# Performance work log

Measured on AMD Instinct MI355X. Metric: run time of the kernel, lower is better.

## Reference

```python
import jax, jax.numpy as jnp
import numpy as np

H = 1024   # hidden_size
V = 32000  # output_size (vocab)
S = 4096   # encoder seq_len
L = 1      # n_layers


def setup_inputs() -> dict:
    key = jax.random.key(0)
    ks = jax.random.split(key, 12)
    scale = 0.02
    return {
        "word_input": jax.random.randint(ks[0], (1,), 0, V),
        "last_hidden": jax.random.normal(ks[1], (L, 1, H), jnp.float32),
        "encoder_hiddens": jax.random.normal(ks[2], (S, 1, H), jnp.float32),
        "embedding": jax.random.normal(ks[3], (V, H), jnp.float32) * scale,
        "w_ih": jax.random.normal(ks[4], (3 * H, H), jnp.float32) * scale,
        "w_hh": jax.random.normal(ks[5], (3 * H, H), jnp.float32) * scale,
        "b_ih": jax.random.normal(ks[6], (3 * H,), jnp.float32) * scale,
        "b_hh": jax.random.normal(ks[7], (3 * H,), jnp.float32) * scale,
        "attn_w": jax.random.normal(ks[8], (H, H), jnp.float32) * scale,
        "attn_b": jax.random.normal(ks[9], (H,), jnp.float32) * scale,
        "out_w": jax.random.normal(ks[10], (V, 2 * H), jnp.float32) * scale,
        "out_b": jax.random.normal(ks[11], (V,), jnp.float32) * scale,
    }


def reference(word_input, last_hidden, encoder_hiddens, embedding,
              w_ih, w_hh, b_ih, b_hh, attn_w, attn_b, out_w, out_b):
    h_dim = embedding.shape[1]
    # embedding lookup -> GRU single step (PyTorch GRU cell math)
    x = embedding[word_input[0]]            # [H]
    h0 = last_hidden[0, 0]                  # [H]
    gx = w_ih @ x + b_ih                    # [3H]
    gh = w_hh @ h0 + b_hh                   # [3H]
    r = jax.nn.sigmoid(gx[:h_dim] + gh[:h_dim])
    z = jax.nn.sigmoid(gx[h_dim:2 * h_dim] + gh[h_dim:2 * h_dim])
    n = jnp.tanh(gx[2 * h_dim:] + r * gh[2 * h_dim:])
    h = (1.0 - z) * n + z * h0              # rnn_output / new hidden [H]
    # Bahdanau-style scores: dot(hidden, attn(enc_i)) for all i, batched
    enc = encoder_hiddens[:, 0, :]          # [S, H]
    scores = (enc @ attn_w.T + attn_b) @ h  # [S]
    attn = jax.nn.softmax(scores)           # [S]
    context = attn @ enc                    # [H]
    output = jnp.concatenate([h, context]) @ out_w.T + out_b  # [V]
    return (output[None, :], h[None, None, :], attn[None, None, :])
```

## Files before the change

### kernel.cpp

```cpp
#include <hip/hip_runtime.h>
#include <cstddef>

#define Hn 1024
#define Vn 32000
#define Sn 4096
#define CSHIFT 20.0f

__device__ __forceinline__ float wave_reduce_sum(float v) {
#pragma unroll
    for (int o = 32; o > 0; o >>= 1) v += __shfl_down(v, o, 64);
    return v;
}


__device__ __forceinline__ void out_h_rows(const float* __restrict__ out_w,
                                           const float* __restrict__ out_b,
                                           const float* __restrict__ ws_h,
                                           float* __restrict__ out,
                                           int row_base, int t)
{
    __shared__ float c[Hn];
    ((float4*)c)[t] = ((const float4*)ws_h)[t];
    __syncthreads();
    const int wv = t >> 6, lane = t & 63;
    const int row = row_base + wv;
    const float* w = out_w + (size_t)row * (2 * Hn);
    float acc = 0.f;
#pragma unroll
    for (int k = 0; k < 4; ++k) {
        const int idx = k * 256 + lane * 4;
        const float4 w4 = *(const float4*)(w + idx);
        acc += w4.x * c[idx] + w4.y * c[idx + 1] + w4.z * c[idx + 2] + w4.w * c[idx + 3];
    }
    acc = wave_reduce_sum(acc);
    if (lane == 0) out[row] = acc + out_b[row];
}

__global__ __launch_bounds__(256) void k_gru(const int* __restrict__ word,
                                             const float* __restrict__ emb,
                                             const float* __restrict__ h0,
                                             const float* __restrict__ w_ih,
                                             const float* __restrict__ w_hh,
                                             const float* __restrict__ b_ih,
                                             const float* __restrict__ b_hh,
                                             float* __restrict__ ws_h,
                                             float* __restrict__ ws_ctx,
                                             float* __restrict__ ws_denom,
                                             float* __restrict__ out_h)
{
    const int k = blockIdx.x;
    const int t = threadIdx.x;

    if (k == 0) {
#pragma unroll
        for (int i = 0; i < 4; ++i) ws_ctx[t + i * 256] = 0.f;
        if (t == 0) ws_denom[0] = 0.f;
    }

    const float* x = emb + (size_t)word[0] * Hn;
    const float4 xv = ((const float4*)x)[t];
    const float4 hv = ((const float4*)h0)[t];

    float acc[6];
    const float* rows[6] = {
        w_ih + (size_t)k * Hn, w_ih + (size_t)(k + Hn) * Hn, w_ih + (size_t)(k + 2 * Hn) * Hn,
        w_hh + (size_t)k * Hn, w_hh + (size_t)(k + Hn) * Hn, w_hh + (size_t)(k + 2 * Hn) * Hn
    };
#pragma unroll
    for (int g = 0; g < 6; ++g) {
        const float4 w = ((const float4*)rows[g])[t];
        const float4 vv = (g < 3) ? xv : hv;
        acc[g] = w.x * vv.x + w.y * vv.y + w.z * vv.z + w.w * vv.w;
    }

    __shared__ float red[6][4];
    const int wv = t >> 6, lane = t & 63;
#pragma unroll
    for (int g = 0; g < 6; ++g) {
        const float s = wave_reduce_sum(acc[g]);
        if (lane == 0) red[g][wv] = s;
    }
    __syncthreads();
    if (t == 0) {
        float g0 = red[0][0] + red[0][1] + red[0][2] + red[0][3] + b_ih[k];
        float g1 = red[1][0] + red[1][1] + red[1][2] + red[1][3] + b_ih[k + Hn];
        float g2 = red[2][0] + red[2][1] + red[2][2] + red[2][3] + b_ih[k + 2 * Hn];
        float g3 = red[3][0] + red[3][1] + red[3][2] + red[3][3] + b_hh[k];
        float g4 = red[4][0] + red[4][1] + red[4][2] + red[4][3] + b_hh[k + Hn];
        float g5 = red[5][0] + red[5][1] + red[5][2] + red[5][3] + b_hh[k + 2 * Hn];
        float r = 1.f / (1.f + expf(-(g0 + g3)));
        float z = 1.f / (1.f + expf(-(g1 + g4)));
        float n = tanhf(g2 + r * g5);
        float hk = (1.f - z) * n + z * h0[k];
        ws_h[k]  = hk;
        out_h[k] = hk;
    }
}

__global__ __launch_bounds__(256) void k_a(const float* __restrict__ attn_w,
                                           const float* __restrict__ ws_h,
                                           float* __restrict__ v,
                                           const float* __restrict__ out_w,
                                           const float* __restrict__ out_b,
                                           float* __restrict__ out)
{
    const int t = threadIdx.x, bid = blockIdx.x;
    if (bid < 64) {
        const int tj = t >> 4, tk = t & 15;
        const int k = bid * 16 + tk;
        float acc = 0.f;
        for (int j = tj; j < Hn; j += 16)
            acc += attn_w[(size_t)j * Hn + k] * ws_h[j];
        __shared__ float p[16][17];
        p[tj][tk] = acc;
        __syncthreads();
        if (t < 16) {
            float s = 0.f;
#pragma unroll
            for (int j = 0; j < 16; ++j) s += p[j][t];
            v[bid * 16 + t] = s;
        }
    } else {
        out_h_rows(out_w, out_b, ws_h, out, (bid - 64) * 4, t);
    }
}

__global__ __launch_bounds__(256) void k_sctx(const float* __restrict__ enc,
                                              const float* __restrict__ ws_v,
                                              float* __restrict__ escore,
                                              float* __restrict__ ctx,
                                              float* __restrict__ denom,
                                              const float* __restrict__ ws_h,
                                              const float* __restrict__ out_w,
                                              const float* __restrict__ out_b,
                                              float* __restrict__ out)
{
    const int t = threadIdx.x, bid = blockIdx.x;
    if (bid < 128) {
        __shared__ float rows[4][Hn];
        __shared__ float vsh[Hn];
        __shared__ float esl[4];
        const int wv = t >> 6, lane = t & 63;
        const int s0 = bid * 32;

        ((float4*)vsh)[t] = ((const float4*)ws_v)[t];

        float4 acc = make_float4(0.f, 0.f, 0.f, 0.f);
        float dsum = 0.f;

        for (int g = 0; g < 8; ++g) {
            __syncthreads();
            const float* erow = enc + (size_t)(s0 + g * 4) * Hn;
#pragma unroll
            for (int r = 0; r < 4; ++r)
                ((float4*)rows[r])[t] = ((const float4*)(erow + (size_t)r * Hn))[t];
            __syncthreads();

            float a = 0.f;
#pragma unroll
            for (int k = 0; k < 4; ++k) {
                const int idx = k * 256 + lane * 4;
                const float4 e = *(const float4*)&rows[wv][idx];
                a += e.x * vsh[idx] + e.y * vsh[idx + 1] + e.z * vsh[idx + 2] + e.w * vsh[idx + 3];
            }
            a = wave_reduce_sum(a);
            if (lane == 0) {
                const float ev = expf(a - CSHIFT);
                esl[wv] = ev;
                escore[s0 + g * 4 + wv] = ev;
            }
            __syncthreads();

            const float e0 = esl[0], e1 = esl[1], e2 = esl[2], e3 = esl[3];
            dsum += e0 + e1 + e2 + e3;
            const float4 r0 = ((const float4*)rows[0])[t];
            const float4 r1 = ((const float4*)rows[1])[t];
            const float4 r2 = ((const float4*)rows[2])[t];
            const float4 r3 = ((const float4*)rows[3])[t];
            acc.x += e0 * r0.x + e1 * r1.x + e2 * r2.x + e3 * r3.x;
            acc.y += e0 * r0.y + e1 * r1.y + e2 * r2.y + e3 * r3.y;
            acc.z += e0 * r0.z + e1 * r1.z + e2 * r2.z + e3 * r3.z;
            acc.w += e0 * r0.w + e1 * r1.w + e2 * r2.w + e3 * r3.w;
        }
        atomicAdd(&ctx[t * 4],     acc.x);
        atomicAdd(&ctx[t * 4 + 1], acc.y);
        atomicAdd(&ctx[t * 4 + 2], acc.z);
        atomicAdd(&ctx[t * 4 + 3], acc.w);
        if (t == 0) atomicAdd(denom, dsum);
    } else {
        out_h_rows(out_w, out_b, ws_h, out, 10668 + (bid - 128) * 4, t);
    }
}

__global__ __launch_bounds__(256) void k_red(const float* __restrict__ escore,
                                             const float* __restrict__ denom,
                                             float* __restrict__ out_attn,
                                             const float* __restrict__ ws_h,
                                             const float* __restrict__ out_w,
                                             const float* __restrict__ out_b,
                                             float* __restrict__ out)
{
    const int t = threadIdx.x, bid = blockIdx.x;
    if (bid < 4) {
        const float inv = 1.f / denom[0];
        const int s = bid * 1024 + t * 4;
        const float4 e = *(const float4*)(escore + s);
        *(float4*)(out_attn + s) = make_float4(e.x * inv, e.y * inv, e.z * inv, e.w * inv);
    } else {
        out_h_rows(out_w, out_b, ws_h, out, 21336 + (bid - 4) * 4, t);
    }
}

__global__ __launch_bounds__(256) void k_tail(const float* __restrict__ out_w,
                                              const float* __restrict__ ws_ctx,
                                              const float* __restrict__ denom,
                                              float* __restrict__ out)
{
    __shared__ float c[Hn];
    const int t = threadIdx.x;
    const float inv = 1.f / denom[0];
    ((float4*)c)[t] = ((const float4*)ws_ctx)[t];
    __syncthreads();
    const int wv = t >> 6, lane = t & 63;
    const int row = blockIdx.x * 4 + wv;
    const float* w = out_w + (size_t)row * (2 * Hn) + Hn;
    float acc = 0.f;
#pragma unroll
    for (int k = 0; k < 4; ++k) {
        const int idx = k * 256 + lane * 4;
        const float4 w4 = *(const float4*)(w + idx);
        acc += w4.x * c[idx] + w4.y * c[idx + 1] + w4.z * c[idx + 2] + w4.w * c[idx + 3];
    }
    acc = wave_reduce_sum(acc);
    if (lane == 0) out[row] += acc * inv;
}

extern "C" void kernel_launch(void* const* d_in, const int* in_sizes, int n_in,
                              void* d_out, int out_size, void* d_ws, size_t ws_size,
                              hipStream_t stream) {
    const int*   word   = (const int*)d_in[0];
    const float* h_last = (const float*)d_in[1];
    const float* enc    = (const float*)d_in[2];
    const float* emb    = (const float*)d_in[3];
    const float* w_ih   = (const float*)d_in[4];
    const float* w_hh   = (const float*)d_in[5];
    const float* b_ih   = (const float*)d_in[6];
    const float* b_hh   = (const float*)d_in[7];
    const float* attn_w = (const float*)d_in[8];
    const float* out_w  = (const float*)d_in[10];
    const float* out_b  = (const float*)d_in[11];
    float* out = (float*)d_out;
    float* ws  = (float*)d_ws;

    float* ws_h      = ws;
    float* ws_ctx    = ws + 1024;
    float* ws_v      = ws + 2048;
    float* ws_escore = ws + 3072;
    float* ws_denom  = ws + 7168;
    float* out_h     = out + Vn;
    float* out_attn  = out + Vn + Hn;

    k_gru<<<Hn, 256, 0, stream>>>(word, emb, h_last, w_ih, w_hh, b_ih, b_hh,
                                  ws_h, ws_ctx, ws_denom, out_h);
    k_a<<<64 + 2667, 256, 0, stream>>>(attn_w, ws_h, ws_v, out_w, out_b, out);
    k_sctx<<<128 + 2667, 256, 0, stream>>>(enc, ws_v, ws_escore, ws_ctx, ws_denom,
                                           ws_h, out_w, out_b, out);
    k_red<<<4 + 2666, 256, 0, stream>>>(ws_escore, ws_denom, out_attn,
                                        ws_h, out_w, out_b, out);
    k_tail<<<Vn / 4, 256, 0, stream>>>(out_w, ws_ctx, ws_denom, out);
}
```

Measured before the change: 95.21 us.

## Merge attention, score/context and normalize kernels into one with atomic-counter dependencies

Three launches (attn projection, score+context, softmax normalize), each padded with out_w h-half rows, become a single kernel. Ordering between the stages now comes from global atomic counters with spin-waits instead of kernel boundaries. The aim is to remove two launch gaps and let the out_w h-half GEMV fill the GPU alongside the dependent attention stages. Spin-waiting blocks assume the producer blocks (lower block IDs) are already resident, which carries a deadlock/ordering risk that relies on in-order dispatch.

```diff
diff --git a/kernel.cpp b/kernel.cpp
--- a/kernel.cpp
+++ b/kernel.cpp
@@ -12,29 +12,20 @@
     return v;
 }
 
-
-__device__ __forceinline__ void out_h_rows(const float* __restrict__ out_w,
-                                           const float* __restrict__ out_b,
-                                           const float* __restrict__ ws_h,
-                                           float* __restrict__ out,
-                                           int row_base, int t)
-{
-    __shared__ float c[Hn];
-    ((float4*)c)[t] = ((const float4*)ws_h)[t];
-    __syncthreads();
-    const int wv = t >> 6, lane = t & 63;
-    const int row = row_base + wv;
-    const float* w = out_w + (size_t)row * (2 * Hn);
-    float acc = 0.f;
-#pragma unroll
-    for (int k = 0; k < 4; ++k) {
-        const int idx = k * 256 + lane * 4;
-        const float4 w4 = *(const float4*)(w + idx);
-        acc += w4.x * c[idx] + w4.y * c[idx + 1] + w4.z * c[idx + 2] + w4.w * c[idx + 3];
-    }
-    acc = wave_reduce_sum(acc);
-    if (lane == 0) out[row] = acc + out_b[row];
-}
+__device__ __forceinline__ void block_signal(int* cnt, int t) {
+    __threadfence();
+    __syncthreads();
+    if (t == 0) __hip_atomic_fetch_add(cnt, 1, __ATOMIC_RELEASE, __HIP_MEMORY_SCOPE_AGENT);
+}
+__device__ __forceinline__ void block_wait(const int* cnt, int target, int t) {
+    if (t == 0) {
+        while (__hip_atomic_load(cnt, __ATOMIC_ACQUIRE, __HIP_MEMORY_SCOPE_AGENT) < target)
+            __builtin_amdgcn_s_sleep(4);
+    }
+    __syncthreads();
+    __threadfence();
+}
+
 
 __global__ __launch_bounds__(256) void k_gru(const int* __restrict__ word,
                                              const float* __restrict__ emb,
@@ -46,6 +37,7 @@
                                              float* __restrict__ ws_h,
                                              float* __restrict__ ws_ctx,
                                              float* __restrict__ ws_denom,
+                                             int*   __restrict__ ws_cnt,
                                              float* __restrict__ out_h)
 {
     const int k = blockIdx.x;
@@ -54,7 +46,7 @@
     if (k == 0) {
 #pragma unroll
         for (int i = 0; i < 4; ++i) ws_ctx[t + i * 256] = 0.f;
-        if (t == 0) ws_denom[0] = 0.f;
+        if (t == 0) { ws_denom[0] = 0.f; ws_cnt[0] = 0; ws_cnt[1] = 0; }
     }
 
     const float* x = emb + (size_t)word[0] * Hn;
@@ -97,51 +89,44 @@
     }
 }
 
-__global__ __launch_bounds__(256) void k_a(const float* __restrict__ attn_w,
-                                           const float* __restrict__ ws_h,
-                                           float* __restrict__ v,
-                                           const float* __restrict__ out_w,
-                                           const float* __restrict__ out_b,
-                                           float* __restrict__ out)
+__global__ __launch_bounds__(256) void k_mid(const float* __restrict__ attn_w,
+                                             const float* __restrict__ enc,
+                                             const float* __restrict__ ws_h,
+                                             float* __restrict__ ws_v,
+                                             float* __restrict__ escore,
+                                             float* __restrict__ ctx,
+                                             float* __restrict__ denom,
+                                             int*   __restrict__ cnt,
+                                             float* __restrict__ out_attn,
+                                             const float* __restrict__ out_w,
+                                             const float* __restrict__ out_b,
+                                             float* __restrict__ out)
 {
+    __shared__ float smem[5128];
     const int t = threadIdx.x, bid = blockIdx.x;
+    const int wv = t >> 6, lane = t & 63;
+
     if (bid < 64) {
         const int tj = t >> 4, tk = t & 15;
         const int k = bid * 16 + tk;
         float acc = 0.f;
         for (int j = tj; j < Hn; j += 16)
             acc += attn_w[(size_t)j * Hn + k] * ws_h[j];
-        __shared__ float p[16][17];
-        p[tj][tk] = acc;
+        smem[tj * 17 + tk] = acc;
         __syncthreads();
         if (t < 16) {
             float s = 0.f;
 #pragma unroll
-            for (int j = 0; j < 16; ++j) s += p[j][t];
-            v[bid * 16 + t] = s;
+            for (int j = 0; j < 16; ++j) s += smem[j * 17 + t];
+            ws_v[bid * 16 + t] = s;
         }
-    } else {
-        out_h_rows(out_w, out_b, ws_h, out, (bid - 64) * 4, t);
-    }
-}
-
-__global__ __launch_bounds__(256) void k_sctx(const float* __restrict__ enc,
-                                              const float* __restrict__ ws_v,
-                                              float* __restrict__ escore,
-                                              float* __restrict__ ctx,
-                                              float* __restrict__ denom,
-                                              const float* __restrict__ ws_h,
-                                              const float* __restrict__ out_w,
-                                              const float* __restrict__ out_b,
-                                              float* __restrict__ out)
-{
-    const int t = threadIdx.x, bid = blockIdx.x;
-    if (bid < 128) {
-        __shared__ float rows[4][Hn];
-        __shared__ float vsh[Hn];
-        __shared__ float esl[4];
-        const int wv = t >> 6, lane = t & 63;
-        const int s0 = bid * 32;
+        block_signal(&cnt[0], t);
+    } else if (bid < 192) {
+        block_wait(&cnt[0], 64, t);
+        float* rows = smem;
+        float* vsh  = smem + 4096;
+        float* esl  = smem + 5120;
+        const int s0 = (bid - 64) * 32;
 
         ((float4*)vsh)[t] = ((const float4*)ws_v)[t];
 
@@ -153,14 +138,14 @@
             const float* erow = enc + (size_t)(s0 + g * 4) * Hn;
 #pragma unroll
             for (int r = 0; r < 4; ++r)
-                ((float4*)rows[r])[t] = ((const float4*)(erow + (size_t)r * Hn))[t];
+                ((float4*)(rows + r * Hn))[t] = ((const float4*)(erow + (size_t)r * Hn))[t];
             __syncthreads();
 
             float a = 0.f;
 #pragma unroll
             for (int k = 0; k < 4; ++k) {
                 const int idx = k * 256 + lane * 4;
-                const float4 e = *(const float4*)&rows[wv][idx];
+                const float4 e = *(const float4*)(rows + wv * Hn + idx);
                 a += e.x * vsh[idx] + e.y * vsh[idx + 1] + e.z * vsh[idx + 2] + e.w * vsh[idx + 3];
             }
             a = wave_reduce_sum(a);
@@ -173,10 +158,10 @@
 
             const float e0 = esl[0], e1 = esl[1], e2 = esl[2], e3 = esl[3];
             dsum += e0 + e1 + e2 + e3;
-            const float4 r0 = ((const float4*)rows[0])[t];
-            const float4 r1 = ((const float4*)rows[1])[t];
-            const float4 r2 = ((const float4*)rows[2])[t];
-            const float4 r3 = ((const float4*)rows[3])[t];
+            const float4 r0 = ((const float4*)(rows))[t];
+            const float4 r1 = ((const float4*)(rows + Hn))[t];
+            const float4 r2 = ((const float4*)(rows + 2 * Hn))[t];
+            const float4 r3 = ((const float4*)(rows + 3 * Hn))[t];
             acc.x += e0 * r0.x + e1 * r1.x + e2 * r2.x + e3 * r3.x;
             acc.y += e0 * r0.y + e1 * r1.y + e2 * r2.y + e3 * r3.y;
             acc.z += e0 * r0.z + e1 * r1.z + e2 * r2.z + e3 * r3.z;
@@ -187,27 +172,28 @@
         atomicAdd(&ctx[t * 4 + 2], acc.z);
         atomicAdd(&ctx[t * 4 + 3], acc.w);
         if (t == 0) atomicAdd(denom, dsum);
-    } else {
-        out_h_rows(out_w, out_b, ws_h, out, 10668 + (bid - 128) * 4, t);
-    }
-}
-
-__global__ __launch_bounds__(256) void k_red(const float* __restrict__ escore,
-                                             const float* __restrict__ denom,
-                                             float* __restrict__ out_attn,
-                                             const float* __restrict__ ws_h,
-                                             const float* __restrict__ out_w,
-                                             const float* __restrict__ out_b,
-                                             float* __restrict__ out)
-{
-    const int t = threadIdx.x, bid = blockIdx.x;
-    if (bid < 4) {
+        block_signal(&cnt[1], t);
+    } else if (bid < 196) {
+        block_wait(&cnt[1], 128, t);
         const float inv = 1.f / denom[0];
-        const int s = bid * 1024 + t * 4;
+        const int s = (bid - 192) * 1024 + t * 4;
         const float4 e = *(const float4*)(escore + s);
         *(float4*)(out_attn + s) = make_float4(e.x * inv, e.y * inv, e.z * inv, e.w * inv);
     } else {
-        out_h_rows(out_w, out_b, ws_h, out, 21336 + (bid - 4) * 4, t);
+        float* c = smem;
+        ((float4*)c)[t] = ((const float4*)ws_h)[t];
+        __syncthreads();
+        const int row = (bid - 196) * 4 + wv;
+        const float* w = out_w + (size_t)row * (2 * Hn);
+        float acc = 0.f;
+#pragma unroll
+        for (int k = 0; k < 4; ++k) {
+            const int idx = k * 256 + lane * 4;
+            const float4 w4 = *(const float4*)(w + idx);
+            acc += w4.x * c[idx] + w4.y * c[idx + 1] + w4.z * c[idx + 2] + w4.w * c[idx + 3];
+        }
+        acc = wave_reduce_sum(acc);
+        if (lane == 0) out[row] = acc + out_b[row];
     }
 }
 
@@ -257,15 +243,13 @@
     float* ws_v      = ws + 2048;
     float* ws_escore = ws + 3072;
     float* ws_denom  = ws + 7168;
+    int*   ws_cnt    = (int*)(ws + 7176);
     float* out_h     = out + Vn;
     float* out_attn  = out + Vn + Hn;
 
     k_gru<<<Hn, 256, 0, stream>>>(word, emb, h_last, w_ih, w_hh, b_ih, b_hh,
-                                  ws_h, ws_ctx, ws_denom, out_h);
-    k_a<<<64 + 2667, 256, 0, stream>>>(attn_w, ws_h, ws_v, out_w, out_b, out);
-    k_sctx<<<128 + 2667, 256, 0, stream>>>(enc, ws_v, ws_escore, ws_ctx, ws_denom,
-                                           ws_h, out_w, out_b, out);
-    k_red<<<4 + 2666, 256, 0, stream>>>(ws_escore, ws_denom, out_attn,
-                                        ws_h, out_w, out_b, out);
+                                  ws_h, ws_ctx, ws_denom, ws_cnt, out_h);
+    k_mid<<<196 + Vn / 4, 256, 0, stream>>>(attn_w, enc, ws_h, ws_v, ws_escore, ws_ctx,
+                                            ws_denom, ws_cnt, out_attn, out_w, out_b, out);
     k_tail<<<Vn / 4, 256, 0, stream>>>(out_w, ws_ctx, ws_denom, out);
 }
```

New measurement: 150.7 us. 1.58x slower.

## Merge attention normalize into tail kernel and rebalance out_w h-rows across kernels

Applied to the files above, without the earlier changes.

Cuts the pipeline from five launches to four by folding the attn normalization into the tail kernel. The attn_w^T·h product becomes row-coalesced float4 loads accumulated with atomics into a pre-zeroed ws_v. The score/context kernel now reads encoder rows directly from global memory instead of staging them through shared memory with per-group barriers. The out_w h-half rows are redistributed: 23000 rows overlap with the attn_w kernel and 9000 with the score kernel. This trades one launch and some sync overhead for extra atomics and a second global read of each encoder row.

```diff
diff --git a/kernel.cpp b/kernel.cpp
--- a/kernel.cpp
+++ b/kernel.cpp
@@ -17,9 +17,9 @@
                                            const float* __restrict__ out_b,
                                            const float* __restrict__ ws_h,
                                            float* __restrict__ out,
+                                           float* __restrict__ c,
                                            int row_base, int t)
 {
-    __shared__ float c[Hn];
     ((float4*)c)[t] = ((const float4*)ws_h)[t];
     __syncthreads();
     const int wv = t >> 6, lane = t & 63;
@@ -45,6 +45,7 @@
                                              const float* __restrict__ b_hh,
                                              float* __restrict__ ws_h,
                                              float* __restrict__ ws_ctx,
+                                             float* __restrict__ ws_v,
                                              float* __restrict__ ws_denom,
                                              float* __restrict__ out_h)
 {
@@ -53,7 +54,10 @@
 
     if (k == 0) {
 #pragma unroll
-        for (int i = 0; i < 4; ++i) ws_ctx[t + i * 256] = 0.f;
+        for (int i = 0; i < 4; ++i) {
+            ws_ctx[t + i * 256] = 0.f;
+            ws_v[t + i * 256]   = 0.f;
+        }
         if (t == 0) ws_denom[0] = 0.f;
     }
 
@@ -104,102 +108,98 @@
                                            const float* __restrict__ out_b,
                                            float* __restrict__ out)
 {
-    const int t = threadIdx.x, bid = blockIdx.x;
-    if (bid < 64) {
-        const int tj = t >> 4, tk = t & 15;
-        const int k = bid * 16 + tk;
-        float acc = 0.f;
-        for (int j = tj; j < Hn; j += 16)
-            acc += attn_w[(size_t)j * Hn + k] * ws_h[j];
-        __shared__ float p[16][17];
-        p[tj][tk] = acc;
-        __syncthreads();
-        if (t < 16) {
-            float s = 0.f;
-#pragma unroll
-            for (int j = 0; j < 16; ++j) s += p[j][t];
-            v[bid * 16 + t] = s;
-        }
-    } else {
-        out_h_rows(out_w, out_b, ws_h, out, (bid - 64) * 4, t);
-    }
-}
-
-__global__ __launch_bounds__(256) void k_sctx(const float* __restrict__ enc,
-                                              const float* __restrict__ ws_v,
-                                              float* __restrict__ escore,
-                                              float* __restrict__ ctx,
-                                              float* __restrict__ denom,
-                                              const float* __restrict__ ws_h,
-                                              const float* __restrict__ out_w,
-                                              const float* __restrict__ out_b,
-                                              float* __restrict__ out)
-{
+    __shared__ float c[Hn];
     const int t = threadIdx.x, bid = blockIdx.x;
     if (bid < 128) {
-        __shared__ float rows[4][Hn];
-        __shared__ float vsh[Hn];
-        __shared__ float esl[4];
+        const int j0 = bid * 8;
+        float4 acc = make_float4(0.f, 0.f, 0.f, 0.f);
+#pragma unroll
+        for (int r = 0; r < 8; ++r) {
+            const int j = j0 + r;
+            const float hj = ws_h[j];
+            const float4 w4 = ((const float4*)(attn_w + (size_t)j * Hn))[t];
+            acc.x += hj * w4.x; acc.y += hj * w4.y;
+            acc.z += hj * w4.z; acc.w += hj * w4.w;
+        }
+        atomicAdd(&v[t * 4],     acc.x);
+        atomicAdd(&v[t * 4 + 1], acc.y);
+        atomicAdd(&v[t * 4 + 2], acc.z);
+        atomicAdd(&v[t * 4 + 3], acc.w);
+    } else {
+        out_h_rows(out_w, out_b, ws_h, out, c, (bid - 128) * 4, t);
+    }
+}
+
+__global__ __launch_bounds__(256) void k_b(const float* __restrict__ enc,
+                                           const float* __restrict__ ws_v,
+                                           float* __restrict__ escore,
+                                           float* __restrict__ ctx,
+                                           float* __restrict__ denom,
+                                           const float* __restrict__ ws_h,
+                                           const float* __restrict__ out_w,
+                                           const float* __restrict__ out_b,
+                                           float* __restrict__ out)
+{
+    __shared__ float smem[Hn];
+    __shared__ float esl[32];
+    const int t = threadIdx.x, bid = blockIdx.x;
+    if (bid < 128) {
         const int wv = t >> 6, lane = t & 63;
         const int s0 = bid * 32;
 
-        ((float4*)vsh)[t] = ((const float4*)ws_v)[t];
-
-        float4 acc = make_float4(0.f, 0.f, 0.f, 0.f);
-        float dsum = 0.f;
-
-        for (int g = 0; g < 8; ++g) {
-            __syncthreads();
-            const float* erow = enc + (size_t)(s0 + g * 4) * Hn;
-#pragma unroll
-            for (int r = 0; r < 4; ++r)
-                ((float4*)rows[r])[t] = ((const float4*)(erow + (size_t)r * Hn))[t];
-            __syncthreads();
-
+        ((float4*)smem)[t] = ((const float4*)ws_v)[t];
+        __syncthreads();
+
+#pragma unroll
+        for (int q = 0; q < 8; ++q) {
+            const int r = wv * 8 + q;
+            const float* row = enc + (size_t)(s0 + r) * Hn;
             float a = 0.f;
 #pragma unroll
             for (int k = 0; k < 4; ++k) {
                 const int idx = k * 256 + lane * 4;
-                const float4 e = *(const float4*)&rows[wv][idx];
-                a += e.x * vsh[idx] + e.y * vsh[idx + 1] + e.z * vsh[idx + 2] + e.w * vsh[idx + 3];
+                const float4 e = *(const float4*)(row + idx);
+                a += e.x * smem[idx] + e.y * smem[idx + 1] + e.z * smem[idx + 2] + e.w * smem[idx + 3];
             }
             a = wave_reduce_sum(a);
             if (lane == 0) {
                 const float ev = expf(a - CSHIFT);
-                esl[wv] = ev;
-                escore[s0 + g * 4 + wv] = ev;
+                esl[r] = ev;
+                escore[s0 + r] = ev;
             }
-            __syncthreads();
-
-            const float e0 = esl[0], e1 = esl[1], e2 = esl[2], e3 = esl[3];
-            dsum += e0 + e1 + e2 + e3;
-            const float4 r0 = ((const float4*)rows[0])[t];
-            const float4 r1 = ((const float4*)rows[1])[t];
-            const float4 r2 = ((const float4*)rows[2])[t];
-            const float4 r3 = ((const float4*)rows[3])[t];
-            acc.x += e0 * r0.x + e1 * r1.x + e2 * r2.x + e3 * r3.x;
-            acc.y += e0 * r0.y + e1 * r1.y + e2 * r2.y + e3 * r3.y;
-            acc.z += e0 * r0.z + e1 * r1.z + e2 * r2.z + e3 * r3.z;
-            acc.w += e0 * r0.w + e1 * r1.w + e2 * r2.w + e3 * r3.w;
+        }
+        __syncthreads();
+
+        float4 acc = make_float4(0.f, 0.f, 0.f, 0.f);
+#pragma unroll 4
+        for (int s = 0; s < 32; ++s) {
+            const float a = esl[s];
+            const float4 e = ((const float4*)(enc + (size_t)(s0 + s) * Hn))[t];
+            acc.x += a * e.x; acc.y += a * e.y; acc.z += a * e.z; acc.w += a * e.w;
         }
         atomicAdd(&ctx[t * 4],     acc.x);
         atomicAdd(&ctx[t * 4 + 1], acc.y);
         atomicAdd(&ctx[t * 4 + 2], acc.z);
         atomicAdd(&ctx[t * 4 + 3], acc.w);
-        if (t == 0) atomicAdd(denom, dsum);
+        if (t == 0) {
+            float d = 0.f;
+#pragma unroll
+            for (int s = 0; s < 32; ++s) d += esl[s];
+            atomicAdd(denom, d);
+        }
     } else {
-        out_h_rows(out_w, out_b, ws_h, out, 10668 + (bid - 128) * 4, t);
-    }
-}
-
-__global__ __launch_bounds__(256) void k_red(const float* __restrict__ escore,
-                                             const float* __restrict__ denom,
-                                             float* __restrict__ out_attn,
-                                             const float* __restrict__ ws_h,
-                                             const float* __restrict__ out_w,
-                                             const float* __restrict__ out_b,
-                                             float* __restrict__ out)
-{
+        out_h_rows(out_w, out_b, ws_h, out, smem, 23000 + (bid - 128) * 4, t);
+    }
+}
+
+__global__ __launch_bounds__(256) void k_tail(const float* __restrict__ out_w,
+                                              const float* __restrict__ ws_ctx,
+                                              const float* __restrict__ escore,
+                                              const float* __restrict__ denom,
+                                              float* __restrict__ out_attn,
+                                              float* __restrict__ out)
+{
+    __shared__ float c[Hn];
     const int t = threadIdx.x, bid = blockIdx.x;
     if (bid < 4) {
         const float inv = 1.f / denom[0];
@@ -207,32 +207,22 @@
         const float4 e = *(const float4*)(escore + s);
         *(float4*)(out_attn + s) = make_float4(e.x * inv, e.y * inv, e.z * inv, e.w * inv);
     } else {
-        out_h_rows(out_w, out_b, ws_h, out, 21336 + (bid - 4) * 4, t);
-    }
-}
-
-__global__ __launch_bounds__(256) void k_tail(const float* __restrict__ out_w,
-                                              const float* __restrict__ ws_ctx,
-                                              const float* __restrict__ denom,
-                                              float* __restrict__ out)
-{
-    __shared__ float c[Hn];
-    const int t = threadIdx.x;
-    const float inv = 1.f / denom[0];
-    ((float4*)c)[t] = ((const float4*)ws_ctx)[t];
-    __syncthreads();
-    const int wv = t >> 6, lane = t & 63;
-    const int row = blockIdx.x * 4 + wv;
-    const float* w = out_w + (size_t)row * (2 * Hn) + Hn;
-    float acc = 0.f;
-#pragma unroll
-    for (int k = 0; k < 4; ++k) {
-        const int idx = k * 256 + lane * 4;
-        const float4 w4 = *(const float4*)(w + idx);
-        acc += w4.x * c[idx] + w4.y * c[idx + 1] + w4.z * c[idx + 2] + w4.w * c[idx + 3];
-    }
-    acc = wave_reduce_sum(acc);
-    if (lane == 0) out[row] += acc * inv;
+        const float inv = 1.f / denom[0];
+        ((float4*)c)[t] = ((const float4*)ws_ctx)[t];
+        __syncthreads();
+        const int wv = t >> 6, lane = t & 63;
+        const int row = (bid - 4) * 4 + wv;
+        const float* w = out_w + (size_t)row * (2 * Hn) + Hn;
+        float acc = 0.f;
+#pragma unroll
+        for (int k = 0; k < 4; ++k) {
+            const int idx = k * 256 + lane * 4;
+            const float4 w4 = *(const float4*)(w + idx);
+            acc += w4.x * c[idx] + w4.y * c[idx + 1] + w4.z * c[idx + 2] + w4.w * c[idx + 3];
+        }
+        acc = wave_reduce_sum(acc);
+        if (lane == 0) out[row] += acc * inv;
+    }
 }
 
 extern "C" void kernel_launch(void* const* d_in, const int* in_sizes, int n_in,
@@ -261,11 +251,10 @@
     float* out_attn  = out + Vn + Hn;
 
     k_gru<<<Hn, 256, 0, stream>>>(word, emb, h_last, w_ih, w_hh, b_ih, b_hh,
-                                  ws_h, ws_ctx, ws_denom, out_h);
-    k_a<<<64 + 2667, 256, 0, stream>>>(attn_w, ws_h, ws_v, out_w, out_b, out);
-    k_sctx<<<128 + 2667, 256, 0, stream>>>(enc, ws_v, ws_escore, ws_ctx, ws_denom,
-                                           ws_h, out_w, out_b, out);
-    k_red<<<4 + 2666, 256, 0, stream>>>(ws_escore, ws_denom, out_attn,
+                                  ws_h, ws_ctx, ws_v, ws_denom, out_h);
+    k_a<<<128 + 5750, 256, 0, stream>>>(attn_w, ws_h, ws_v, out_w, out_b, out);
+    k_b<<<128 + 2250, 256, 0, stream>>>(enc, ws_v, ws_escore, ws_ctx, ws_denom,
                                         ws_h, out_w, out_b, out);
-    k_tail<<<Vn / 4, 256, 0, stream>>>(out_w, ws_ctx, ws_denom, out);
-}
+    k_tail<<<4 + Vn / 4, 256, 0, stream>>>(out_w, ws_ctx, ws_escore, ws_denom,
+                                           out_attn, out);
+}
```

Result: faster. 84.59 us (-11.2%).
